# Kernel optimization log

Hardware: AMD Instinct MI355X
Metric: run time of the kernel (lower is better)

## Reference

```python
import jax, jax.numpy as jnp
import numpy as np

T = 16384
D_IN = 512
D_HID = 512
D_OUT = 512


def setup_inputs() -> dict:
    key = jax.random.key(0)
    ks = jax.random.split(key, 7)
    s_in = 1.0 / np.sqrt(D_IN)
    s_hid = 1.0 / np.sqrt(D_HID)
    xs = jax.random.normal(ks[0], (T, D_IN), dtype=jnp.float32)
    Wz = jax.random.uniform(ks[1], (D_HID, D_IN), jnp.float32, -s_in, s_in)
    bz = jax.random.uniform(ks[2], (D_HID,), jnp.float32, -s_in, s_in)
    Wh = jax.random.uniform(ks[3], (D_HID, D_IN), jnp.float32, -s_in, s_in)
    bh = jax.random.uniform(ks[4], (D_HID,), jnp.float32, -s_in, s_in)
    Wo = jax.random.uniform(ks[5], (D_OUT, D_HID), jnp.float32, -s_hid, s_hid)
    bo = jax.random.uniform(ks[6], (D_OUT,), jnp.float32, -s_hid, s_hid)
    return {"xs": xs, "Wz": Wz, "bz": bz, "Wh": Wh, "bh": bh, "Wo": Wo, "bo": bo}


def _combine(first, second):
    a0, b0 = first
    a1, b1 = second
    return (a0 * a1, a1 * b0 + b1)


def reference(xs, Wz, bz, Wh, bh, Wo, bo):
    # gates and candidate hidden states: [T, H]
    zs = jax.nn.sigmoid(xs @ Wz.T + bz)
    hs = xs @ Wh.T + bh
    # prepend identity element (a=1, b=0) for the h_0 = 0 initial state
    a = jnp.concatenate([jnp.ones((1, zs.shape[1]), zs.dtype), 1.0 - zs], axis=0)
    b = jnp.concatenate([jnp.zeros((1, zs.shape[1]), zs.dtype), zs * hs], axis=0)
    _, states = jax.lax.associative_scan(_combine, (a, b))  # [T+1, H]
    return states[1:] @ Wo.T + bo  # [T, D_OUT]
```

## Files before the change

kernel.cpp:

```cpp
#include <hip/hip_runtime.h>
#include <hip/hip_bf16.h>
#include <cstdint>
#include <cmath>

#define T_SEQ 16384
#define DMODEL 512
#define NCHUNK 512
#define LCHUNK 32
#define W_N    (DMODEL * DMODEL)
#define N4_W   (W_N / 4)
#define N4_W3  (3 * N4_W)
#define BK     32
#define NT     (DMODEL / BK)

typedef __bf16 bf16x8 __attribute__((ext_vector_type(8)));
typedef float  f32x4  __attribute__((ext_vector_type(4)));

using bf16 = __hip_bfloat16;

__device__ __forceinline__ void load_lds16(const void* g, void* l) {
    __builtin_amdgcn_global_load_lds((const __attribute__((address_space(1))) void*)g,
                                     (__attribute__((address_space(3))) void*)l,
                                     16, 0, 0);
}

__device__ __forceinline__ unsigned short f2bf(float f) {
    union { float f; unsigned u; } v; v.f = f;
    const unsigned r = (v.u + 0x7FFFu + ((v.u >> 16) & 1u)) >> 16;
    return (unsigned short)r;
}
__device__ __forceinline__ float bf2f(unsigned short u) {
    union { unsigned u; float f; } v; v.u = ((unsigned)u) << 16;
    return v.f;
}

__device__ __forceinline__ void comb(float& A, float& B, float fA, float fB,
                                     float sA, float sB) {
    A = fA * sA;
    B = sA * fB + sB;
}

__global__ __launch_bounds__(256) void k_convert_w(
    const float* __restrict__ Wz, const float* __restrict__ Wh,
    const float* __restrict__ Wo,
    bf16* __restrict__ Wz_c, bf16* __restrict__ Wh_c, bf16* __restrict__ Wo_c)
{
    const int i = blockIdx.x * 256 + threadIdx.x;
    if (i >= N4_W3) return;
    const int w = i >> 16;
    const int o = i & 65535;
    const float* src = (w == 0) ? Wz : (w == 1) ? Wh : Wo;
    bf16* dst = (w == 0) ? Wz_c : (w == 1) ? Wh_c : Wo_c;
    const float4 v = ((const float4*)src)[o];
    ushort4 r;
    r.x = f2bf(v.x); r.y = f2bf(v.y); r.z = f2bf(v.z); r.w = f2bf(v.w);
    ((ushort4*)dst)[o] = r;
}

__global__ __launch_bounds__(256, 2) void gemm_zh(
    const float* __restrict__ xs, const bf16* __restrict__ Wz, const float* __restrict__ bz,
    const bf16* __restrict__ Wh, const float* __restrict__ bh,
    unsigned int* __restrict__ ab_ws,
    float* __restrict__ AaggT, float* __restrict__ BaggT)
{
    __shared__ __bf16 As[2][128 * BK];
    __shared__ __bf16 Zs[2][128 * BK];
    __shared__ __bf16 Hs[2][128 * BK];

    const int tid  = threadIdx.x;
    const int bm   = blockIdx.x;
    const int bn   = blockIdx.y;
    const int lane = tid & 63;
    const int wave = tid >> 6;
    const int wm   = wave >> 1;
    const int wn   = wave & 1;
    const int quad = lane >> 4;
    const int col  = lane & 15;

    f32x4 accz[4][4], acch[4][4];
    #pragma unroll
    for (int i = 0; i < 4; ++i)
        #pragma unroll
        for (int j = 0; j < 4; ++j) {
            accz[i][j] = (f32x4){0.f, 0.f, 0.f, 0.f};
            acch[i][j] = (f32x4){0.f, 0.f, 0.f, 0.f};
        }

    const int wrow = tid >> 2;
    const int wq   = (tid & 3) ^ ((tid >> 3) & 3);
    const bf16* zg = Wz + (size_t)(bn * 128 + wrow) * DMODEL + wq * 8;
    const bf16* hg = Wh + (size_t)(bn * 128 + wrow) * DMODEL + wq * 8;

    const int frow = tid >> 3;
    const int f4   = tid & 7;
    const float* xg = xs + ((size_t)(bm * 128) + frow) * DMODEL + f4 * 4;
    const int xoff = frow * BK + ((((f4 >> 1) ^ ((frow >> 1) & 3))) << 3) + (f4 & 1) * 4;

    const int fq = quad ^ ((col >> 1) & 3);
    int offA[4], offB[4];
    #pragma unroll
    for (int i = 0; i < 4; ++i) {
        offA[i] = (wm * 64 + i * 16 + col) * BK + fq * 8;
        offB[i] = (wn * 64 + i * 16 + col) * BK + fq * 8;
    }

    float4 xr[4];

    auto XLOAD = [&](int t) {
        const int k0 = t * BK;
        #pragma unroll
        for (int it = 0; it < 4; ++it)
            xr[it] = *(const float4*)(xg + (size_t)(it * 32) * DMODEL + k0);
    };
    auto STAGE_W = [&](int t, int p) {
        const int k0 = t * BK;
        #pragma unroll
        for (int it = 0; it < 2; ++it) {
            const int chunk = it * 256 + tid;
            load_lds16(zg + (size_t)(it * 64) * DMODEL + k0, &Zs[p][chunk * 8]);
            load_lds16(hg + (size_t)(it * 64) * DMODEL + k0, &Hs[p][chunk * 8]);
        }
    };
    auto XWRITE = [&](int p) {
        #pragma unroll
        for (int it = 0; it < 4; ++it) {
            __hip_bfloat162 p0 = __float22bfloat162_rn(make_float2(xr[it].x, xr[it].y));
            __hip_bfloat162 p1 = __float22bfloat162_rn(make_float2(xr[it].z, xr[it].w));
            uint2 pk;
            pk.x = *(const unsigned*)&p0;
            pk.y = *(const unsigned*)&p1;
            *(uint2*)&As[p][xoff + it * 32 * BK] = pk;
        }
    };
    auto COMPUTE = [&](int p) {
        bf16x8 af[4], zf[4], hf[4];
        #pragma unroll
        for (int i = 0; i < 4; ++i) {
            af[i] = *(const bf16x8*)&As[p][offA[i]];
            zf[i] = *(const bf16x8*)&Zs[p][offB[i]];
            hf[i] = *(const bf16x8*)&Hs[p][offB[i]];
        }
        #pragma unroll
        for (int i = 0; i < 4; ++i)
            #pragma unroll
            for (int j = 0; j < 4; ++j) {
                accz[i][j] = __builtin_amdgcn_mfma_f32_16x16x32_bf16(af[i], zf[j], accz[i][j], 0, 0, 0);
                acch[i][j] = __builtin_amdgcn_mfma_f32_16x16x32_bf16(af[i], hf[j], acch[i][j], 0, 0, 0);
            }
    };

    XLOAD(0); STAGE_W(0, 0); XWRITE(0);
    __syncthreads();
    for (int t = 0; t < NT - 1; ++t) {
        const int p = t & 1;
        XLOAD(t + 1);
        STAGE_W(t + 1, p ^ 1);
        COMPUTE(p);
        XWRITE(p ^ 1);
        __syncthreads();
    }
    COMPUTE((NT - 1) & 1);

    const int c_lo = bm * 4 + wm * 2;
    #pragma unroll
    for (int j = 0; j < 4; ++j) {
        const int n = bn * 128 + wn * 64 + j * 16 + col;
        const float bzv = bz[n];
        const float bhv = bh[n];
        float cA[4], cB[4];
        #pragma unroll
        for (int i = 0; i < 4; ++i) {
            const int mbase = bm * 128 + wm * 64 + i * 16 + quad * 4;
            float A = 1.f, B = 0.f;
            #pragma unroll
            for (int r = 0; r < 4; ++r) {
                const float zpre = accz[i][j][r] + bzv;
                const float hpre = acch[i][j][r] + bhv;
                const float z = 1.f / (1.f + __expf(-zpre));
                const float a = 1.f - z;
                const float b = z * hpre;
                const size_t idx = (size_t)(mbase + r) * DMODEL + n;
                ab_ws[idx] = (unsigned)f2bf(a) | ((unsigned)f2bf(b) << 16);
                A = a * A;
                B = a * B + b;
            }
            cA[i] = A; cB[i] = B;
        }
        #pragma unroll
        for (int i = 0; i < 4; ++i) {
            float pA = __shfl_xor(cA[i], 16);
            float pB = __shfl_xor(cB[i], 16);
            const bool hi1 = quad & 1;
            comb(cA[i], cB[i], hi1 ? pA : cA[i], hi1 ? pB : cB[i],
                               hi1 ? cA[i] : pA, hi1 ? cB[i] : pB);
            pA = __shfl_xor(cA[i], 32);
            pB = __shfl_xor(cB[i], 32);
            const bool hi2 = quad >> 1;
            comb(cA[i], cB[i], hi2 ? pA : cA[i], hi2 ? pB : cB[i],
                               hi2 ? cA[i] : pA, hi2 ? cB[i] : pB);
        }
        float Alo, Blo, Ahi, Bhi;
        comb(Alo, Blo, cA[0], cB[0], cA[1], cB[1]);
        comb(Ahi, Bhi, cA[2], cB[2], cA[3], cB[3]);
        if (quad == 0) {
            AaggT[(size_t)n * NCHUNK + c_lo]     = Alo;
            BaggT[(size_t)n * NCHUNK + c_lo]     = Blo;
            AaggT[(size_t)n * NCHUNK + c_lo + 1] = Ahi;
            BaggT[(size_t)n * NCHUNK + c_lo + 1] = Bhi;
        }
    }
}

__global__ __launch_bounds__(512) void scan_p2(
    const float* __restrict__ AaggT, const float* __restrict__ BaggT,
    float* __restrict__ HpreT)
{
    const int h = blockIdx.x;
    const int c = threadIdx.x;
    __shared__ float sA[NCHUNK], sB[NCHUNK];

    float A = AaggT[(size_t)h * NCHUNK + c];
    float B = BaggT[(size_t)h * NCHUNK + c];
    sA[c] = A; sB[c] = B;
    __syncthreads();

    for (int off = 1; off < NCHUNK; off <<= 1) {
        float pA = 1.f, pB = 0.f;
        if (c >= off) { pA = sA[c - off]; pB = sB[c - off]; }
        __syncthreads();
        const float nB = A * pB + B;
        const float nA = A * pA;
        A = nA; B = nB;
        sA[c] = A; sB[c] = B;
        __syncthreads();
    }
    const float hp = (c == 0) ? 0.f : sB[c - 1];
    HpreT[(size_t)h * NCHUNK + c] = hp;
}

__global__ __launch_bounds__(256) void scan_p3(
    const unsigned int* __restrict__ ab_ws, const float* __restrict__ HpreT,
    unsigned short* __restrict__ states)
{
    const int tid = threadIdx.x;
    const int c   = blockIdx.x;
    const int ch  = blockIdx.y * 256 + tid;
    float H = HpreT[(size_t)ch * NCHUNK + c];
    const size_t base = (size_t)(c * LCHUNK) * DMODEL + ch;
    #pragma unroll 8
    for (int i = 0; i < LCHUNK; ++i) {
        const unsigned u = ab_ws[base + (size_t)i * DMODEL];
        const float a = bf2f((unsigned short)(u & 0xFFFFu));
        const float b = bf2f((unsigned short)(u >> 16));
        H = a * H + b;
        states[base + (size_t)i * DMODEL] = f2bf(H);
    }
}

__global__ __launch_bounds__(256, 2) void gemm_out(
    const bf16* __restrict__ states, const bf16* __restrict__ Wo, const float* __restrict__ bo,
    float* __restrict__ out)
{
    __shared__ __bf16 As[2][128 * BK];
    __shared__ __bf16 Bs[2][128 * BK];

    const int tid  = threadIdx.x;
    const int bm   = blockIdx.x;
    const int bn   = blockIdx.y;
    const int lane = tid & 63;
    const int wave = tid >> 6;
    const int wm   = wave >> 1;
    const int wn   = wave & 1;
    const int quad = lane >> 4;
    const int col  = lane & 15;

    f32x4 acc[4][4];
    #pragma unroll
    for (int i = 0; i < 4; ++i)
        #pragma unroll
        for (int j = 0; j < 4; ++j)
            acc[i][j] = (f32x4){0.f, 0.f, 0.f, 0.f};

    const int wrow = tid >> 2;
    const int wq   = (tid & 3) ^ ((tid >> 3) & 3);
    const bf16* ag = states + (size_t)(bm * 128 + wrow) * DMODEL + wq * 8;
    const bf16* bg = Wo     + (size_t)(bn * 128 + wrow) * DMODEL + wq * 8;

    const int fq = quad ^ ((col >> 1) & 3);
    int offA[4], offB[4];
    #pragma unroll
    for (int i = 0; i < 4; ++i) {
        offA[i] = (wm * 64 + i * 16 + col) * BK + fq * 8;
        offB[i] = (wn * 64 + i * 16 + col) * BK + fq * 8;
    }

    auto STAGE = [&](int t, int p) {
        const int k0 = t * BK;
        #pragma unroll
        for (int it = 0; it < 2; ++it) {
            const int chunk = it * 256 + tid;
            load_lds16(ag + (size_t)(it * 64) * DMODEL + k0, &As[p][chunk * 8]);
            load_lds16(bg + (size_t)(it * 64) * DMODEL + k0, &Bs[p][chunk * 8]);
        }
    };
    auto COMPUTE = [&](int p) {
        bf16x8 af[4], bf[4];
        #pragma unroll
        for (int i = 0; i < 4; ++i) {
            af[i] = *(const bf16x8*)&As[p][offA[i]];
            bf[i] = *(const bf16x8*)&Bs[p][offB[i]];
        }
        #pragma unroll
        for (int i = 0; i < 4; ++i)
            #pragma unroll
            for (int j = 0; j < 4; ++j)
                acc[i][j] = __builtin_amdgcn_mfma_f32_16x16x32_bf16(af[i], bf[j], acc[i][j], 0, 0, 0);
    };

    STAGE(0, 0);
    __syncthreads();
    for (int t = 0; t < NT - 1; ++t) {
        const int p = t & 1;
        STAGE(t + 1, p ^ 1);
        COMPUTE(p);
        __syncthreads();
    }
    COMPUTE((NT - 1) & 1);

    #pragma unroll
    for (int j = 0; j < 4; ++j) {
        const int n = bn * 128 + wn * 64 + j * 16 + col;
        const float bov = bo[n];
        #pragma unroll
        for (int i = 0; i < 4; ++i) {
            const int mbase = bm * 128 + wm * 64 + i * 16 + quad * 4;
            #pragma unroll
            for (int r = 0; r < 4; ++r)
                out[(size_t)(mbase + r) * DMODEL + n] = acc[i][j][r] + bov;
        }
    }
}

extern "C" void kernel_launch(void* const* d_in, const int* in_sizes, int n_in,
                              void* d_out, int out_size, void* d_ws, size_t ws_size,
                              hipStream_t stream)
{
    const float* xs = (const float*)d_in[0];
    const float* Wz = (const float*)d_in[1];
    const float* bz = (const float*)d_in[2];
    const float* Wh = (const float*)d_in[3];
    const float* bh = (const float*)d_in[4];
    const float* Wo = (const float*)d_in[5];
    const float* bo = (const float*)d_in[6];
    float* out = (float*)d_out;

    char* w = (char*)d_ws;
    bf16*  Wz_c   = (bf16*) (w);
    bf16*  Wh_c   = (bf16*) (w + 524288ull);
    bf16*  Wo_c   = (bf16*) (w + 1048576ull);
    unsigned int*   ab_ws  = (unsigned int*)  (w + 1572864ull);
    unsigned short* states = (unsigned short*)(w + 35127296ull);
    float* AaggT  = (float*)(w + 51904512ull);
    float* BaggT  = (float*)(w + 52953088ull);
    float* HpreT  = (float*)(w + 54001664ull);

    k_convert_w<<<(N4_W3 + 255) / 256, 256, 0, stream>>>(Wz, Wh, Wo, Wz_c, Wh_c, Wo_c);
    gemm_zh<<<dim3(128, 4), 256, 0, stream>>>(xs, Wz_c, bz, Wh_c, bh, ab_ws, AaggT, BaggT);
    scan_p2<<<DMODEL, NCHUNK, 0, stream>>>(AaggT, BaggT, HpreT);
    scan_p3<<<dim3(NCHUNK, 2), 256, 0, stream>>>(ab_ws, HpreT, states);
    gemm_out<<<dim3(128, 4), 256, 0, stream>>>((const bf16*)states, Wo_c, bo, out);
}
```

Baseline: 167.4 us.

## Pre-convert xs to bf16 and triple-buffer LDS pipelines in both GEMMs

Converts xs to bf16 in the existing conversion kernel, writing it into the states buffer, so gemm_zh can stage the activation tile straight into LDS with global_load_lds instead of loading fp32 through registers and converting. Both GEMMs move from double to triple buffering, with explicit vmcnt waits and one barrier per k-step, so loads run two tiles ahead of compute. The cost is an extra full pass over xs (read fp32, write bf16) in a separate kernel, plus more LDS per block, which may reduce occupancy; gemm_out's launch bound is raised to 3.

```diff
diff --git a/kernel.cpp b/kernel.cpp
--- a/kernel.cpp
+++ b/kernel.cpp
@@ -10,6 +10,8 @@
 #define W_N    (DMODEL * DMODEL)
 #define N4_W   (W_N / 4)
 #define N4_W3  (3 * N4_W)
+#define N4_X   (T_SEQ * DMODEL / 4)
+#define N4_ALL (N4_W3 + N4_X)
 #define BK     32
 #define NT     (DMODEL / BK)
 
@@ -40,17 +42,23 @@
     B = sA * fB + sB;
 }
 
-__global__ __launch_bounds__(256) void k_convert_w(
+__global__ __launch_bounds__(256) void k_convert(
+    const float* __restrict__ xs,
     const float* __restrict__ Wz, const float* __restrict__ Wh,
     const float* __restrict__ Wo,
-    bf16* __restrict__ Wz_c, bf16* __restrict__ Wh_c, bf16* __restrict__ Wo_c)
+    bf16* __restrict__ xs_c, bf16* __restrict__ Wz_c,
+    bf16* __restrict__ Wh_c, bf16* __restrict__ Wo_c)
 {
     const int i = blockIdx.x * 256 + threadIdx.x;
-    if (i >= N4_W3) return;
-    const int w = i >> 16;
-    const int o = i & 65535;
-    const float* src = (w == 0) ? Wz : (w == 1) ? Wh : Wo;
-    bf16* dst = (w == 0) ? Wz_c : (w == 1) ? Wh_c : Wo_c;
+    if (i >= N4_ALL) return;
+    const float* src; bf16* dst; int o;
+    if (i < N4_W3) {
+        const int w = i >> 16; o = i & 65535;
+        src = (w == 0) ? Wz : (w == 1) ? Wh : Wo;
+        dst = (w == 0) ? Wz_c : (w == 1) ? Wh_c : Wo_c;
+    } else {
+        o = i - N4_W3; src = xs; dst = xs_c;
+    }
     const float4 v = ((const float4*)src)[o];
     ushort4 r;
     r.x = f2bf(v.x); r.y = f2bf(v.y); r.z = f2bf(v.z); r.w = f2bf(v.w);
@@ -58,14 +66,14 @@
 }
 
 __global__ __launch_bounds__(256, 2) void gemm_zh(
-    const float* __restrict__ xs, const bf16* __restrict__ Wz, const float* __restrict__ bz,
+    const bf16* __restrict__ xs_c, const bf16* __restrict__ Wz, const float* __restrict__ bz,
     const bf16* __restrict__ Wh, const float* __restrict__ bh,
     unsigned int* __restrict__ ab_ws,
     float* __restrict__ AaggT, float* __restrict__ BaggT)
 {
-    __shared__ __bf16 As[2][128 * BK];
-    __shared__ __bf16 Zs[2][128 * BK];
-    __shared__ __bf16 Hs[2][128 * BK];
+    __shared__ __bf16 As[3][128 * BK];
+    __shared__ __bf16 Zs[3][128 * BK];
+    __shared__ __bf16 Hs[3][128 * BK];
 
     const int tid  = threadIdx.x;
     const int bm   = blockIdx.x;
@@ -88,13 +96,9 @@
 
     const int wrow = tid >> 2;
     const int wq   = (tid & 3) ^ ((tid >> 3) & 3);
-    const bf16* zg = Wz + (size_t)(bn * 128 + wrow) * DMODEL + wq * 8;
-    const bf16* hg = Wh + (size_t)(bn * 128 + wrow) * DMODEL + wq * 8;
-
-    const int frow = tid >> 3;
-    const int f4   = tid & 7;
-    const float* xg = xs + ((size_t)(bm * 128) + frow) * DMODEL + f4 * 4;
-    const int xoff = frow * BK + ((((f4 >> 1) ^ ((frow >> 1) & 3))) << 3) + (f4 & 1) * 4;
+    const bf16* ag = xs_c + (size_t)(bm * 128 + wrow) * DMODEL + wq * 8;
+    const bf16* zg = Wz   + (size_t)(bn * 128 + wrow) * DMODEL + wq * 8;
+    const bf16* hg = Wh   + (size_t)(bn * 128 + wrow) * DMODEL + wq * 8;
 
     const int fq = quad ^ ((col >> 1) & 3);
     int offA[4], offB[4];
@@ -104,32 +108,14 @@
         offB[i] = (wn * 64 + i * 16 + col) * BK + fq * 8;
     }
 
-    float4 xr[4];
-
-    auto XLOAD = [&](int t) {
-        const int k0 = t * BK;
-        #pragma unroll
-        for (int it = 0; it < 4; ++it)
-            xr[it] = *(const float4*)(xg + (size_t)(it * 32) * DMODEL + k0);
-    };
-    auto STAGE_W = [&](int t, int p) {
+    auto STAGE = [&](int t, int p) {
         const int k0 = t * BK;
         #pragma unroll
         for (int it = 0; it < 2; ++it) {
             const int chunk = it * 256 + tid;
+            load_lds16(ag + (size_t)(it * 64) * DMODEL + k0, &As[p][chunk * 8]);
             load_lds16(zg + (size_t)(it * 64) * DMODEL + k0, &Zs[p][chunk * 8]);
             load_lds16(hg + (size_t)(it * 64) * DMODEL + k0, &Hs[p][chunk * 8]);
-        }
-    };
-    auto XWRITE = [&](int p) {
-        #pragma unroll
-        for (int it = 0; it < 4; ++it) {
-            __hip_bfloat162 p0 = __float22bfloat162_rn(make_float2(xr[it].x, xr[it].y));
-            __hip_bfloat162 p1 = __float22bfloat162_rn(make_float2(xr[it].z, xr[it].w));
-            uint2 pk;
-            pk.x = *(const unsigned*)&p0;
-            pk.y = *(const unsigned*)&p1;
-            *(uint2*)&As[p][xoff + it * 32 * BK] = pk;
         }
     };
     auto COMPUTE = [&](int p) {
@@ -149,17 +135,23 @@
             }
     };
 
-    XLOAD(0); STAGE_W(0, 0); XWRITE(0);
-    __syncthreads();
+    STAGE(0, 0); STAGE(1, 1);
+    int pc = 0;
     for (int t = 0; t < NT - 1; ++t) {
-        const int p = t & 1;
-        XLOAD(t + 1);
-        STAGE_W(t + 1, p ^ 1);
-        COMPUTE(p);
-        XWRITE(p ^ 1);
-        __syncthreads();
-    }
-    COMPUTE((NT - 1) & 1);
+        asm volatile("s_waitcnt vmcnt(6)" ::: "memory");
+        __builtin_amdgcn_s_barrier();
+        __builtin_amdgcn_sched_barrier(0);
+        if (t + 2 < NT) {
+            const int pn = (pc == 0) ? 2 : pc - 1;
+            STAGE(t + 2, pn);
+        }
+        COMPUTE(pc);
+        pc = (pc == 2) ? 0 : pc + 1;
+    }
+    asm volatile("s_waitcnt vmcnt(0)" ::: "memory");
+    __builtin_amdgcn_s_barrier();
+    __builtin_amdgcn_sched_barrier(0);
+    COMPUTE(pc);
 
     const int c_lo = bm * 4 + wm * 2;
     #pragma unroll
@@ -257,12 +249,12 @@
     }
 }
 
-__global__ __launch_bounds__(256, 2) void gemm_out(
+__global__ __launch_bounds__(256, 3) void gemm_out(
     const bf16* __restrict__ states, const bf16* __restrict__ Wo, const float* __restrict__ bo,
     float* __restrict__ out)
 {
-    __shared__ __bf16 As[2][128 * BK];
-    __shared__ __bf16 Bs[2][128 * BK];
+    __shared__ __bf16 As[3][128 * BK];
+    __shared__ __bf16 Bs[3][128 * BK];
 
     const int tid  = threadIdx.x;
     const int bm   = blockIdx.x;
@@ -317,15 +309,23 @@
                 acc[i][j] = __builtin_amdgcn_mfma_f32_16x16x32_bf16(af[i], bf[j], acc[i][j], 0, 0, 0);
     };
 
-    STAGE(0, 0);
-    __syncthreads();
+    STAGE(0, 0); STAGE(1, 1);
+    int pc = 0;
     for (int t = 0; t < NT - 1; ++t) {
-        const int p = t & 1;
-        STAGE(t + 1, p ^ 1);
-        COMPUTE(p);
-        __syncthreads();
-    }
-    COMPUTE((NT - 1) & 1);
+        asm volatile("s_waitcnt vmcnt(4)" ::: "memory");
+        __builtin_amdgcn_s_barrier();
+        __builtin_amdgcn_sched_barrier(0);
+        if (t + 2 < NT) {
+            const int pn = (pc == 0) ? 2 : pc - 1;
+            STAGE(t + 2, pn);
+        }
+        COMPUTE(pc);
+        pc = (pc == 2) ? 0 : pc + 1;
+    }
+    asm volatile("s_waitcnt vmcnt(0)" ::: "memory");
+    __builtin_amdgcn_s_barrier();
+    __builtin_amdgcn_sched_barrier(0);
+    COMPUTE(pc);
 
     #pragma unroll
     for (int j = 0; j < 4; ++j) {
@@ -363,9 +363,10 @@
     float* AaggT  = (float*)(w + 51904512ull);
     float* BaggT  = (float*)(w + 52953088ull);
     float* HpreT  = (float*)(w + 54001664ull);
-
-    k_convert_w<<<(N4_W3 + 255) / 256, 256, 0, stream>>>(Wz, Wh, Wo, Wz_c, Wh_c, Wo_c);
-    gemm_zh<<<dim3(128, 4), 256, 0, stream>>>(xs, Wz_c, bz, Wh_c, bh, ab_ws, AaggT, BaggT);
+    bf16*  xs_c   = (bf16*) states;
+
+    k_convert<<<(N4_ALL + 255) / 256, 256, 0, stream>>>(xs, Wz, Wh, Wo, xs_c, Wz_c, Wh_c, Wo_c);
+    gemm_zh<<<dim3(128, 4), 256, 0, stream>>>(xs_c, Wz_c, bz, Wh_c, bh, ab_ws, AaggT, BaggT);
     scan_p2<<<DMODEL, NCHUNK, 0, stream>>>(AaggT, BaggT, HpreT);
     scan_p3<<<dim3(NCHUNK, 2), 256, 0, stream>>>(ab_ws, HpreT, states);
     gemm_out<<<dim3(128, 4), 256, 0, stream>>>((const bf16*)states, Wo_c, bo, out);
```

New measurement: 151.8 us. 1.1x faster.
